# Kernel optimization log

Hardware: AMD Instinct MI355X
Metric: run time of the kernel (lower is better)

Reference implementation:

```python
import jax, jax.numpy as jnp
import numpy as np

N, F_IN, H, C, G, E = 50000, 128, 4, 64, 512, 800000
NEG_SLOPE = 0.2


def setup_inputs() -> dict:
    key = jax.random.key(0)
    ks = jax.random.split(key, 12)
    s = 0.05
    return {
        "x": jax.random.normal(ks[0], (N, F_IN), jnp.float32),
        "W1": jax.random.normal(ks[1], (F_IN, H * C), jnp.float32) * s,
        "att_src1": jax.random.normal(ks[2], (H, C), jnp.float32) * s,
        "att_dst1": jax.random.normal(ks[3], (H, C), jnp.float32) * s,
        "b1": jnp.zeros((H * C,), jnp.float32),
        "W2": jax.random.normal(ks[4], (H * C, C), jnp.float32) * s,
        "att_src2": jax.random.normal(ks[5], (1, C), jnp.float32) * s,
        "att_dst2": jax.random.normal(ks[6], (1, C), jnp.float32) * s,
        "b2": jnp.zeros((C,), jnp.float32),
        "fc_w": jax.random.normal(ks[7], (C, 1), jnp.float32) * s,
        "fc_b": jnp.zeros((1,), jnp.float32),
        "edge_index": jax.random.randint(ks[8], (2, E), 0, N, dtype=jnp.int64),
        "batch": jnp.sort(jax.random.randint(ks[9], (N,), 0, G, dtype=jnp.int64)),
    }


def gat_conv(x, src, dst, W, att_src, att_dst, bias, heads, ch):
    # PyG GATConv: linear -> per-node attn halves -> per-edge leaky_relu ->
    # segment softmax over incoming edges of dst -> weighted scatter-sum.
    n = x.shape[0]
    h = (x @ W).reshape(n, heads, ch)                       # [N,H,C]
    a_s = (h * att_src[None]).sum(-1)                       # [N,H]
    a_d = (h * att_dst[None]).sum(-1)                       # [N,H]
    alpha = jax.nn.leaky_relu(a_s[src] + a_d[dst], NEG_SLOPE)  # [E,H]
    amax = jax.ops.segment_max(alpha, dst, num_segments=n)
    ex = jnp.exp(alpha - amax[dst])
    denom = jax.ops.segment_sum(ex, dst, num_segments=n)
    w = ex / (denom[dst] + 1e-16)                           # [E,H]
    msg = h[src] * w[..., None]                             # [E,H,C]
    out = jax.ops.segment_sum(msg, dst, num_segments=n)     # [N,H,C]
    return out.reshape(n, heads * ch) + bias


def reference(x, W1, att_src1, att_dst1, b1, W2, att_src2, att_dst2, b2,
              fc_w, fc_b, edge_index, batch):
    # add self-loops (PyG GATConv default)
    loops = jnp.arange(N, dtype=edge_index.dtype)
    src = jnp.concatenate([edge_index[0], loops])
    dst = jnp.concatenate([edge_index[1], loops])
    h = jax.nn.relu(gat_conv(x, src, dst, W1, att_src1, att_dst1, b1, H, C))
    h = jax.nn.relu(gat_conv(h, src, dst, W2, att_src2, att_dst2, b2, 1, C))
    cnt = jax.ops.segment_sum(jnp.ones((N,), h.dtype), batch, num_segments=G)
    pooled = jax.ops.segment_sum(h, batch, num_segments=G) / jnp.maximum(cnt, 1.0)[:, None]
    return (pooled @ fc_w + fc_b)[:, 0]                      # [G]
```

## Files before the change

kernel.cpp:

```cpp
#include <hip/hip_runtime.h>
#include <hip/hip_fp16.h>
#include <math.h>

#define NN 50000
#define FIN 128
#define HH 4
#define CC 64
#define HC (HH*CC)
#define GG 512
#define EE 800000
#define ET (EE + NN)
#define NEG_SLOPE 0.2f
#define SCAN_NB 196

typedef _Float16 half8 __attribute__((ext_vector_type(8)));
typedef _Float16 half4 __attribute__((ext_vector_type(4)));
typedef float floatx4 __attribute__((ext_vector_type(4)));

__device__ __forceinline__ float waveReduceSum(float v) {
    #pragma unroll
    for (int off = 32; off > 0; off >>= 1) v += __shfl_xor(v, off);
    return v;
}

__global__ __launch_bounds__(256) void init0_kernel(int* __restrict__ counts,
                                                    const float* __restrict__ W1,
                                                    const float* __restrict__ W2,
                                                    __half* __restrict__ W1t,
                                                    __half* __restrict__ W2t) {
    int i = blockIdx.x * 256 + threadIdx.x;
    int stride = gridDim.x * 256;
    for (int j = i; j < NN + GG; j += stride) counts[j] = 0;
    for (int j = i; j < HC * FIN; j += stride) {
        int n = j >> 7, k = j & 127;
        W1t[j] = __float2half(W1[(size_t)k * HC + n]);
    }
    for (int j = i; j < CC * HC; j += stride) {
        int n = j >> 8, k = j & 255;
        W2t[j] = __float2half(W2[(size_t)k * CC + n]);
    }
}

__global__ __launch_bounds__(256) void histcnt_kernel(const int* __restrict__ ei,
                                                      int* __restrict__ counts,
                                                      const int* __restrict__ batch,
                                                      int* __restrict__ gcnt) {
    int e = blockIdx.x * 256 + threadIdx.x;
    if (e < ET) {
        int d = (e < EE) ? ei[EE + e] : e - EE;
        atomicAdd(&counts[d], 1);
    }
    if (e < NN) atomicAdd(&gcnt[batch[e]], 1);
}

__global__ __launch_bounds__(256) void scanA_kernel(const int* __restrict__ counts,
                                                    int* __restrict__ bsum) {
    __shared__ int sh[256];
    int t = threadIdx.x;
    int i = blockIdx.x * 256 + t;
    sh[t] = (i < NN) ? counts[i] : 0;
    __syncthreads();
    #pragma unroll
    for (int off = 128; off > 0; off >>= 1) {
        if (t < off) sh[t] += sh[t + off];
        __syncthreads();
    }
    if (t == 0) bsum[blockIdx.x] = sh[0];
}

__global__ __launch_bounds__(512) void scanB_kernel(int* __restrict__ bsum,
                                                    const int* __restrict__ gcnt,
                                                    int* __restrict__ gptr) {
    __shared__ int sh[512];
    int t = threadIdx.x;
    int v = (t < SCAN_NB) ? bsum[t] : 0;
    sh[t] = v;
    __syncthreads();
    for (int off = 1; off < 512; off <<= 1) {
        int u = (t >= off) ? sh[t - off] : 0;
        __syncthreads();
        sh[t] += u;
        __syncthreads();
    }
    if (t < SCAN_NB) bsum[t] = sh[t] - v;
    __syncthreads();
    int g = gcnt[t];
    sh[t] = g;
    __syncthreads();
    for (int off = 1; off < 512; off <<= 1) {
        int u = (t >= off) ? sh[t - off] : 0;
        __syncthreads();
        sh[t] += u;
        __syncthreads();
    }
    gptr[t] = sh[t] - g;
    if (t == 511) gptr[512] = sh[t];
}

__global__ __launch_bounds__(256) void scanC_kernel(const int* __restrict__ counts,
                                                    const int* __restrict__ bsum,
                                                    int* __restrict__ rowptr,
                                                    int* __restrict__ cursor) {
    __shared__ int sh[256];
    int t = threadIdx.x;
    int i = blockIdx.x * 256 + t;
    int v = (i < NN) ? counts[i] : 0;
    sh[t] = v;
    __syncthreads();
    for (int off = 1; off < 256; off <<= 1) {
        int u = (t >= off) ? sh[t - off] : 0;
        __syncthreads();
        sh[t] += u;
        __syncthreads();
    }
    int excl = sh[t] - v + bsum[blockIdx.x];
    if (i < NN) { rowptr[i] = excl; cursor[i] = excl; }
    if (i == NN - 1) rowptr[NN] = excl + v;
}

__global__ __launch_bounds__(256) void fill_kernel(const int* __restrict__ ei,
                                                   int* __restrict__ cursor,
                                                   int* __restrict__ scsr) {
    int e = blockIdx.x * 256 + threadIdx.x;
    if (e >= ET) return;
    int s, d;
    if (e < EE) { s = ei[e]; d = ei[EE + e]; } else { s = d = e - EE; }
    int pos = atomicAdd(&cursor[d], 1);
    scsr[pos] = s;
}

__global__ __launch_bounds__(256) void gemm1_mfma_kernel(
    const float* __restrict__ x, const __half* __restrict__ W1t,
    const float* __restrict__ att_src1, const float* __restrict__ att_dst1,
    __half* __restrict__ h1, float* __restrict__ a_s1, float* __restrict__ a_d1)
{
    __shared__ __align__(16) float xs[32][FIN + 4];
    int t = threadIdx.x;
    int n0 = blockIdx.x * 32;
    #pragma unroll
    for (int i = 0; i < 4; ++i) {
        int idx = t + i * 256;
        int row = idx >> 5, c4 = idx & 31;
        int m = n0 + row; if (m >= NN) m = NN - 1;
        float4 v = *(const float4*)(x + (size_t)m * FIN + c4 * 4);
        *(float4*)&xs[row][c4 * 4] = v;
    }
    __syncthreads();

    int w = t >> 6;
    int l = t & 63;
    int nbase = n0 + (w >> 1) * 16;
    int chalf = (w & 1) * 128;
    int lm = l & 15, lb = l >> 4;
    int lrow = (w >> 1) * 16 + lm;

    half8 afrag[4];
    #pragma unroll
    for (int q = 0; q < 4; ++q) {
        float4 lo = *(const float4*)&xs[lrow][q * 32 + lb * 8];
        float4 hi = *(const float4*)&xs[lrow][q * 32 + lb * 8 + 4];
        half8 f;
        #pragma unroll
        for (int i = 0; i < 4; ++i) {
            f[i] = (_Float16)(&lo.x)[i];
            f[4 + i] = (_Float16)(&hi.x)[i];
        }
        afrag[q] = f;
    }
    floatx4 acc[8];
    #pragma unroll
    for (int tt = 0; tt < 8; ++tt) acc[tt] = (floatx4){0.f, 0.f, 0.f, 0.f};

    const __half* wt = W1t + (size_t)(chalf + lm) * FIN + lb * 8;
    #pragma unroll
    for (int tt = 0; tt < 8; ++tt) {
        const __half* wtt = wt + (size_t)tt * 16 * FIN;
        #pragma unroll
        for (int q = 0; q < 4; ++q) {
            half8 b = *(const half8*)(wtt + q * 32);
            acc[tt] = __builtin_amdgcn_mfma_f32_16x16x32_f16(afrag[q], b, acc[tt], 0, 0, 0);
        }
    }
    #pragma unroll
    for (int hh = 0; hh < 2; ++hh) {
        float as_p[4] = {0.f, 0.f, 0.f, 0.f};
        float ad_p[4] = {0.f, 0.f, 0.f, 0.f};
        #pragma unroll
        for (int tt = 0; tt < 4; ++tt) {
            int ti = hh * 4 + tt;
            int col = chalf + ti * 16 + lm;
            float asw = att_src1[col], adw = att_dst1[col];
            #pragma unroll
            for (int r = 0; r < 4; ++r) {
                int n = nbase + lb * 4 + r;
                float v = acc[ti][r];
                if (n < NN) h1[(size_t)n * HC + col] = __float2half(v);
                as_p[r] += v * asw;
                ad_p[r] += v * adw;
            }
        }
        #pragma unroll
        for (int off = 1; off < 16; off <<= 1) {
            #pragma unroll
            for (int r = 0; r < 4; ++r) {
                as_p[r] += __shfl_xor(as_p[r], off);
                ad_p[r] += __shfl_xor(ad_p[r], off);
            }
        }
        if (lm == 0) {
            int head = (chalf >> 6) + hh;
            #pragma unroll
            for (int r = 0; r < 4; ++r) {
                int n = nbase + lb * 4 + r;
                if (n < NN) { a_s1[n * HH + head] = as_p[r]; a_d1[n * HH + head] = ad_p[r]; }
            }
        }
    }
}

__global__ __launch_bounds__(256) void emsg1_kernel(
    const int* __restrict__ rowptr, const int* __restrict__ scsr,
    const float* __restrict__ a_s, const float* __restrict__ a_d,
    const half4* __restrict__ h1v, const float* __restrict__ b1,
    half4* __restrict__ out1v)
{
    int d = blockIdx.x * 4 + (threadIdx.x >> 6);
    int l = threadIdx.x & 63;
    int head = l >> 4;
    int start = rowptr[d], end = rowptr[d + 1];
    float ad = a_d[d * HH + head];
    float den = 0.f;
    float a0 = 0.f, a1 = 0.f, a2 = 0.f, a3 = 0.f;
    int j = start;
    for (; j + 3 < end; j += 4) {
        int s0 = scsr[j], s1 = scsr[j + 1], s2 = scsr[j + 2], s3 = scsr[j + 3];
        float e0 = a_s[s0 * HH + head] + ad;
        float e1 = a_s[s1 * HH + head] + ad;
        float e2 = a_s[s2 * HH + head] + ad;
        float e3 = a_s[s3 * HH + head] + ad;
        e0 = (e0 > 0.f) ? e0 : NEG_SLOPE * e0;
        e1 = (e1 > 0.f) ? e1 : NEG_SLOPE * e1;
        e2 = (e2 > 0.f) ? e2 : NEG_SLOPE * e2;
        e3 = (e3 > 0.f) ? e3 : NEG_SLOPE * e3;
        float w0 = __expf(e0), w1 = __expf(e1), w2 = __expf(e2), w3 = __expf(e3);
        half4 v0 = h1v[(size_t)s0 * 64 + l];
        half4 v1 = h1v[(size_t)s1 * 64 + l];
        half4 v2 = h1v[(size_t)s2 * 64 + l];
        half4 v3 = h1v[(size_t)s3 * 64 + l];
        den += (w0 + w1) + (w2 + w3);
        a0 += w0 * (float)v0[0] + w1 * (float)v1[0] + w2 * (float)v2[0] + w3 * (float)v3[0];
        a1 += w0 * (float)v0[1] + w1 * (float)v1[1] + w2 * (float)v2[1] + w3 * (float)v3[1];
        a2 += w0 * (float)v0[2] + w1 * (float)v1[2] + w2 * (float)v2[2] + w3 * (float)v3[2];
        a3 += w0 * (float)v0[3] + w1 * (float)v1[3] + w2 * (float)v2[3] + w3 * (float)v3[3];
    }
    for (; j < end; ++j) {
        int s0 = scsr[j];
        float e0 = a_s[s0 * HH + head] + ad;
        e0 = (e0 > 0.f) ? e0 : NEG_SLOPE * e0;
        float w0 = __expf(e0);
        half4 v0 = h1v[(size_t)s0 * 64 + l];
        den += w0;
        a0 += w0 * (float)v0[0];
        a1 += w0 * (float)v0[1];
        a2 += w0 * (float)v0[2];
        a3 += w0 * (float)v0[3];
    }
    float inv = 1.f / (den + 1e-16f);
    float4 bb = *(const float4*)(b1 + l * 4);
    float r0 = a0 * inv + bb.x; r0 = r0 > 0.f ? r0 : 0.f;
    float r1 = a1 * inv + bb.y; r1 = r1 > 0.f ? r1 : 0.f;
    float r2 = a2 * inv + bb.z; r2 = r2 > 0.f ? r2 : 0.f;
    float r3 = a3 * inv + bb.w; r3 = r3 > 0.f ? r3 : 0.f;
    half4 o;
    o[0] = (_Float16)r0; o[1] = (_Float16)r1; o[2] = (_Float16)r2; o[3] = (_Float16)r3;
    out1v[(size_t)d * 64 + l] = o;
}

__global__ __launch_bounds__(256) void gemm2_mfma_kernel(
    const __half* __restrict__ out1r, const __half* __restrict__ W2t,
    const float* __restrict__ att_src2, const float* __restrict__ att_dst2,
    __half* __restrict__ h2, float* __restrict__ a_s2, float* __restrict__ a_d2)
{
    __shared__ __align__(16) __half ys[64][HC + 8];
    int t = threadIdx.x;
    int n0 = blockIdx.x * 64;
    #pragma unroll
    for (int i = 0; i < 8; ++i) {
        int idx = t + i * 256;
        int row = idx >> 5, c8 = idx & 31;
        int m = n0 + row; if (m >= NN) m = NN - 1;
        *(half8*)&ys[row][c8 * 8] = *(const half8*)(out1r + (size_t)m * HC + c8 * 8);
    }
    __syncthreads();

    int w = t >> 6;
    int l = t & 63;
    int nbase = n0 + w * 16;
    int lm = l & 15, lb = l >> 4;
    int lrow = w * 16 + lm;

    half8 afrag[8];
    #pragma unroll
    for (int q = 0; q < 8; ++q) afrag[q] = *(const half8*)&ys[lrow][q * 32 + lb * 8];

    floatx4 acc[4];
    #pragma unroll
    for (int tt = 0; tt < 4; ++tt) acc[tt] = (floatx4){0.f, 0.f, 0.f, 0.f};

    const __half* wt = W2t + (size_t)lm * HC + lb * 8;
    #pragma unroll
    for (int tt = 0; tt < 4; ++tt) {
        const __half* wtt = wt + (size_t)tt * 16 * HC;
        #pragma unroll
        for (int q = 0; q < 8; ++q) {
            half8 b = *(const half8*)(wtt + q * 32);
            acc[tt] = __builtin_amdgcn_mfma_f32_16x16x32_f16(afrag[q], b, acc[tt], 0, 0, 0);
        }
    }
    float as_p[4] = {0.f, 0.f, 0.f, 0.f};
    float ad_p[4] = {0.f, 0.f, 0.f, 0.f};
    #pragma unroll
    for (int tt = 0; tt < 4; ++tt) {
        int col = tt * 16 + lm;
        float asw = att_src2[col], adw = att_dst2[col];
        #pragma unroll
        for (int r = 0; r < 4; ++r) {
            int n = nbase + lb * 4 + r;
            float v = acc[tt][r];
            if (n < NN) h2[(size_t)n * CC + col] = __float2half(v);
            as_p[r] += v * asw;
            ad_p[r] += v * adw;
        }
    }
    #pragma unroll
    for (int off = 1; off < 16; off <<= 1) {
        #pragma unroll
        for (int r = 0; r < 4; ++r) {
            as_p[r] += __shfl_xor(as_p[r], off);
            ad_p[r] += __shfl_xor(ad_p[r], off);
        }
    }
    if (lm == 0) {
        #pragma unroll
        for (int r = 0; r < 4; ++r) {
            int n = nbase + lb * 4 + r;
            if (n < NN) { a_s2[n] = as_p[r]; a_d2[n] = ad_p[r]; }
        }
    }
}

__global__ __launch_bounds__(256) void emsg2_kernel(
    const int* __restrict__ rowptr, const int* __restrict__ scsr,
    const float* __restrict__ a_s, const float* __restrict__ a_d,
    const half4* __restrict__ h2v, const float* __restrict__ b2,
    const float* __restrict__ fc_w, float* __restrict__ part)
{
    int d = blockIdx.x * 4 + (threadIdx.x >> 6);
    int l = threadIdx.x & 63;
    int u = l & 15;
    int es = l >> 4;
    int start = rowptr[d], end = rowptr[d + 1];
    float ad = a_d[d];
    float den = 0.f;
    float a0 = 0.f, a1 = 0.f, a2 = 0.f, a3 = 0.f;
    int j = start + es;
    for (; j + 4 < end; j += 8) {
        int sA = scsr[j], sB = scsr[j + 4];
        float eA = a_s[sA] + ad;
        float eB = a_s[sB] + ad;
        eA = (eA > 0.f) ? eA : NEG_SLOPE * eA;
        eB = (eB > 0.f) ? eB : NEG_SLOPE * eB;
        float wA = __expf(eA), wB = __expf(eB);
        half4 vA = h2v[(size_t)sA * 16 + u];
        half4 vB = h2v[(size_t)sB * 16 + u];
        den += wA + wB;
        a0 += wA * (float)vA[0] + wB * (float)vB[0];
        a1 += wA * (float)vA[1] + wB * (float)vB[1];
        a2 += wA * (float)vA[2] + wB * (float)vB[2];
        a3 += wA * (float)vA[3] + wB * (float)vB[3];
    }
    if (j < end) {
        int s = scsr[j];
        float e = a_s[s] + ad;
        e = (e > 0.f) ? e : NEG_SLOPE * e;
        float w = __expf(e);
        half4 v = h2v[(size_t)s * 16 + u];
        den += w;
        a0 += w * (float)v[0];
        a1 += w * (float)v[1];
        a2 += w * (float)v[2];
        a3 += w * (float)v[3];
    }
    #pragma unroll
    for (int off = 16; off < 64; off <<= 1) {
        den += __shfl_xor(den, off);
        a0 += __shfl_xor(a0, off);
        a1 += __shfl_xor(a1, off);
        a2 += __shfl_xor(a2, off);
        a3 += __shfl_xor(a3, off);
    }
    float inv = 1.f / (den + 1e-16f);
    float4 bb = *(const float4*)(b2 + u * 4);
    float4 fw = *(const float4*)(fc_w + u * 4);
    float h0 = a0 * inv + bb.x; h0 = h0 > 0.f ? h0 : 0.f;
    float h1 = a1 * inv + bb.y; h1 = h1 > 0.f ? h1 : 0.f;
    float h2 = a2 * inv + bb.z; h2 = h2 > 0.f ? h2 : 0.f;
    float h3 = a3 * inv + bb.w; h3 = h3 > 0.f ? h3 : 0.f;
    float p = h0 * fw.x + h1 * fw.y + h2 * fw.z + h3 * fw.w;
    #pragma unroll
    for (int off = 1; off < 16; off <<= 1) p += __shfl_xor(p, off);
    if (l == 0) part[d] = p;
}

__global__ void pool_kernel(const float* __restrict__ part, const int* __restrict__ gptr,
                            const float* __restrict__ fc_b, float* __restrict__ out)
{
    int g = blockIdx.x;
    int lane = threadIdx.x;
    int start = gptr[g], end = gptr[g + 1];
    float s = 0.f;
    for (int i = start + lane; i < end; i += 64) s += part[i];
    s = waveReduceSum(s);
    if (lane == 0) out[g] = s / fmaxf((float)(end - start), 1.f) + fc_b[0];
}

extern "C" void kernel_launch(void* const* d_in, const int* in_sizes, int n_in,
                              void* d_out, int out_size, void* d_ws, size_t ws_size,
                              hipStream_t stream)
{
    const float* x        = (const float*)d_in[0];
    const float* W1       = (const float*)d_in[1];
    const float* att_src1 = (const float*)d_in[2];
    const float* att_dst1 = (const float*)d_in[3];
    const float* b1       = (const float*)d_in[4];
    const float* W2       = (const float*)d_in[5];
    const float* att_src2 = (const float*)d_in[6];
    const float* att_dst2 = (const float*)d_in[7];
    const float* b2       = (const float*)d_in[8];
    const float* fc_w     = (const float*)d_in[9];
    const float* fc_b     = (const float*)d_in[10];
    const int*   ei       = (const int*)d_in[11];
    const int*   batch    = (const int*)d_in[12];
    float* out = (float*)d_out;

    char* p = (char*)d_ws;
    __half* W1t   = (__half*)p; p += (size_t)HC * FIN * sizeof(__half);
    __half* W2t   = (__half*)p; p += (size_t)CC * HC * sizeof(__half);
    __half* h1    = (__half*)p; p += (size_t)NN * HC * sizeof(__half);
    __half* out1r = (__half*)p; p += (size_t)NN * HC * sizeof(__half);
    __half* h2    = (__half*)p; p += (size_t)NN * CC * sizeof(__half);
    float* a_s1   = (float*)p;  p += (size_t)NN * HH * sizeof(float);
    float* a_d1   = (float*)p;  p += (size_t)NN * HH * sizeof(float);
    float* a_s2   = (float*)p;  p += NN * sizeof(float);
    float* a_d2   = (float*)p;  p += NN * sizeof(float);
    float* part   = (float*)p;  p += NN * sizeof(float);
    int* counts   = (int*)p;    p += NN * sizeof(int);
    int* gcnt     = (int*)p;    p += GG * sizeof(int);
    int* rowptr   = (int*)p;    p += (NN + 1) * sizeof(int);
    int* cursor   = (int*)p;    p += NN * sizeof(int);
    int* scsr     = (int*)p;    p += ET * sizeof(int);
    int* bsum     = (int*)p;    p += SCAN_NB * sizeof(int);
    int* gptr     = (int*)p;    p += (GG + 1) * sizeof(int);

    const int EB = (ET + 255) / 256;

    init0_kernel<<<256, 256, 0, stream>>>(counts, W1, W2, W1t, W2t);
    histcnt_kernel<<<EB, 256, 0, stream>>>(ei, counts, batch, gcnt);
    scanA_kernel<<<SCAN_NB, 256, 0, stream>>>(counts, bsum);
    scanB_kernel<<<1, 512, 0, stream>>>(bsum, gcnt, gptr);
    scanC_kernel<<<SCAN_NB, 256, 0, stream>>>(counts, bsum, rowptr, cursor);
    fill_kernel<<<EB, 256, 0, stream>>>(ei, cursor, scsr);
    gemm1_mfma_kernel<<<(NN + 31) / 32, 256, 0, stream>>>(x, W1t, att_src1, att_dst1,
                                                          h1, a_s1, a_d1);
    emsg1_kernel<<<NN / 4, 256, 0, stream>>>(rowptr, scsr, a_s1, a_d1,
                                             (const half4*)h1, b1, (half4*)out1r);
    gemm2_mfma_kernel<<<(NN + 63) / 64, 256, 0, stream>>>(out1r, W2t, att_src2, att_dst2,
                                                          h2, a_s2, a_d2);
    emsg2_kernel<<<NN / 4, 256, 0, stream>>>(rowptr, scsr, a_s2, a_d2,
                                             (const half4*)h2, b2, fc_w, part);
    pool_kernel<<<GG, 64, 0, stream>>>(part, gptr, fc_b, out);
}
```

Before: 279.5 us.

## Fuse CSR fill into GEMM1 launch and deepen gather unrolling in edge kernels

New measurement: 287.3 us. 1.03x slower.

```diff
diff --git a/kernel.cpp b/kernel.cpp
--- a/kernel.cpp
+++ b/kernel.cpp
@@ -12,6 +12,8 @@
 #define ET (EE + NN)
 #define NEG_SLOPE 0.2f
 #define SCAN_NB 196
+#define GEMM1_NB 1563
+#define EB 3321
 
 typedef _Float16 half8 __attribute__((ext_vector_type(8)));
 typedef _Float16 half4 __attribute__((ext_vector_type(4)));
@@ -118,22 +120,21 @@
     if (i == NN - 1) rowptr[NN] = excl + v;
 }
 
-__global__ __launch_bounds__(256) void fill_kernel(const int* __restrict__ ei,
-                                                   int* __restrict__ cursor,
-                                                   int* __restrict__ scsr) {
-    int e = blockIdx.x * 256 + threadIdx.x;
-    if (e >= ET) return;
-    int s, d;
-    if (e < EE) { s = ei[e]; d = ei[EE + e]; } else { s = d = e - EE; }
-    int pos = atomicAdd(&cursor[d], 1);
-    scsr[pos] = s;
-}
-
-__global__ __launch_bounds__(256) void gemm1_mfma_kernel(
+__global__ __launch_bounds__(256) void fillgemm1_kernel(
+    const int* __restrict__ ei, int* __restrict__ cursor, int* __restrict__ scsr,
     const float* __restrict__ x, const __half* __restrict__ W1t,
     const float* __restrict__ att_src1, const float* __restrict__ att_dst1,
     __half* __restrict__ h1, float* __restrict__ a_s1, float* __restrict__ a_d1)
 {
+    if (blockIdx.x >= GEMM1_NB) {
+        int e = (blockIdx.x - GEMM1_NB) * 256 + threadIdx.x;
+        if (e >= ET) return;
+        int s, d;
+        if (e < EE) { s = ei[e]; d = ei[EE + e]; } else { s = d = e - EE; }
+        int pos = atomicAdd(&cursor[d], 1);
+        scsr[pos] = s;
+        return;
+    }
     __shared__ __align__(16) float xs[32][FIN + 4];
     int t = threadIdx.x;
     int n0 = blockIdx.x * 32;
@@ -232,26 +233,27 @@
     float den = 0.f;
     float a0 = 0.f, a1 = 0.f, a2 = 0.f, a3 = 0.f;
     int j = start;
-    for (; j + 3 < end; j += 4) {
-        int s0 = scsr[j], s1 = scsr[j + 1], s2 = scsr[j + 2], s3 = scsr[j + 3];
-        float e0 = a_s[s0 * HH + head] + ad;
-        float e1 = a_s[s1 * HH + head] + ad;
-        float e2 = a_s[s2 * HH + head] + ad;
-        float e3 = a_s[s3 * HH + head] + ad;
-        e0 = (e0 > 0.f) ? e0 : NEG_SLOPE * e0;
-        e1 = (e1 > 0.f) ? e1 : NEG_SLOPE * e1;
-        e2 = (e2 > 0.f) ? e2 : NEG_SLOPE * e2;
-        e3 = (e3 > 0.f) ? e3 : NEG_SLOPE * e3;
-        float w0 = __expf(e0), w1 = __expf(e1), w2 = __expf(e2), w3 = __expf(e3);
-        half4 v0 = h1v[(size_t)s0 * 64 + l];
-        half4 v1 = h1v[(size_t)s1 * 64 + l];
-        half4 v2 = h1v[(size_t)s2 * 64 + l];
-        half4 v3 = h1v[(size_t)s3 * 64 + l];
-        den += (w0 + w1) + (w2 + w3);
-        a0 += w0 * (float)v0[0] + w1 * (float)v1[0] + w2 * (float)v2[0] + w3 * (float)v3[0];
-        a1 += w0 * (float)v0[1] + w1 * (float)v1[1] + w2 * (float)v2[1] + w3 * (float)v3[1];
-        a2 += w0 * (float)v0[2] + w1 * (float)v1[2] + w2 * (float)v2[2] + w3 * (float)v3[2];
-        a3 += w0 * (float)v0[3] + w1 * (float)v1[3] + w2 * (float)v2[3] + w3 * (float)v3[3];
+    for (; j + 7 < end; j += 8) {
+        int s[8];
+        #pragma unroll
+        for (int q = 0; q < 8; ++q) s[q] = scsr[j + q];
+        float e[8];
+        #pragma unroll
+        for (int q = 0; q < 8; ++q) e[q] = a_s[s[q] * HH + head] + ad;
+        half4 v[8];
+        #pragma unroll
+        for (int q = 0; q < 8; ++q) v[q] = h1v[(size_t)s[q] * 64 + l];
+        #pragma unroll
+        for (int q = 0; q < 8; ++q) {
+            float eq = e[q];
+            eq = (eq > 0.f) ? eq : NEG_SLOPE * eq;
+            float wq = __expf(eq);
+            den += wq;
+            a0 += wq * (float)v[q][0];
+            a1 += wq * (float)v[q][1];
+            a2 += wq * (float)v[q][2];
+            a3 += wq * (float)v[q][3];
+        }
     }
     for (; j < end; ++j) {
         int s0 = scsr[j];
@@ -364,22 +366,29 @@
     float den = 0.f;
     float a0 = 0.f, a1 = 0.f, a2 = 0.f, a3 = 0.f;
     int j = start + es;
-    for (; j + 4 < end; j += 8) {
-        int sA = scsr[j], sB = scsr[j + 4];
-        float eA = a_s[sA] + ad;
-        float eB = a_s[sB] + ad;
-        eA = (eA > 0.f) ? eA : NEG_SLOPE * eA;
-        eB = (eB > 0.f) ? eB : NEG_SLOPE * eB;
-        float wA = __expf(eA), wB = __expf(eB);
-        half4 vA = h2v[(size_t)sA * 16 + u];
-        half4 vB = h2v[(size_t)sB * 16 + u];
-        den += wA + wB;
-        a0 += wA * (float)vA[0] + wB * (float)vB[0];
-        a1 += wA * (float)vA[1] + wB * (float)vB[1];
-        a2 += wA * (float)vA[2] + wB * (float)vB[2];
-        a3 += wA * (float)vA[3] + wB * (float)vB[3];
-    }
-    if (j < end) {
+    for (; j + 12 < end; j += 16) {
+        int s[4];
+        #pragma unroll
+        for (int q = 0; q < 4; ++q) s[q] = scsr[j + q * 4];
+        float e[4];
+        #pragma unroll
+        for (int q = 0; q < 4; ++q) e[q] = a_s[s[q]] + ad;
+        half4 v[4];
+        #pragma unroll
+        for (int q = 0; q < 4; ++q) v[q] = h2v[(size_t)s[q] * 16 + u];
+        #pragma unroll
+        for (int q = 0; q < 4; ++q) {
+            float eq = e[q];
+            eq = (eq > 0.f) ? eq : NEG_SLOPE * eq;
+            float wq = __expf(eq);
+            den += wq;
+            a0 += wq * (float)v[q][0];
+            a1 += wq * (float)v[q][1];
+            a2 += wq * (float)v[q][2];
+            a3 += wq * (float)v[q][3];
+        }
+    }
+    for (; j < end; j += 4) {
         int s = scsr[j];
         float e = a_s[s] + ad;
         e = (e > 0.f) ? e : NEG_SLOPE * e;
@@ -462,16 +471,14 @@
     int* bsum     = (int*)p;    p += SCAN_NB * sizeof(int);
     int* gptr     = (int*)p;    p += (GG + 1) * sizeof(int);
 
-    const int EB = (ET + 255) / 256;
-
     init0_kernel<<<256, 256, 0, stream>>>(counts, W1, W2, W1t, W2t);
     histcnt_kernel<<<EB, 256, 0, stream>>>(ei, counts, batch, gcnt);
     scanA_kernel<<<SCAN_NB, 256, 0, stream>>>(counts, bsum);
     scanB_kernel<<<1, 512, 0, stream>>>(bsum, gcnt, gptr);
     scanC_kernel<<<SCAN_NB, 256, 0, stream>>>(counts, bsum, rowptr, cursor);
-    fill_kernel<<<EB, 256, 0, stream>>>(ei, cursor, scsr);
-    gemm1_mfma_kernel<<<(NN + 31) / 32, 256, 0, stream>>>(x, W1t, att_src1, att_dst1,
-                                                          h1, a_s1, a_d1);
+    fillgemm1_kernel<<<GEMM1_NB + EB, 256, 0, stream>>>(ei, cursor, scsr,
+                                                        x, W1t, att_src1, att_dst1,
+                                                        h1, a_s1, a_d1);
     emsg1_kernel<<<NN / 4, 256, 0, stream>>>(rowptr, scsr, a_s1, a_d1,
                                              (const half4*)h1, b1, (half4*)out1r);
     gemm2_mfma_kernel<<<(NN + 63) / 64, 256, 0, stream>>>(out1r, W2t, att_src2, att_dst2,
```

## Merge CSR-build preprocessing kernels into one cooperative kernel with grid syncs

Applied to the files above, without the earlier changes.

After: 752.6 us. 2.69x slower.

```diff
diff --git a/kernel.cpp b/kernel.cpp
--- a/kernel.cpp
+++ b/kernel.cpp
@@ -1,6 +1,9 @@
 #include <hip/hip_runtime.h>
 #include <hip/hip_fp16.h>
+#include <hip/hip_cooperative_groups.h>
 #include <math.h>
+
+namespace cg = cooperative_groups;
 
 #define NN 50000
 #define FIN 128
@@ -12,6 +15,7 @@
 #define ET (EE + NN)
 #define NEG_SLOPE 0.2f
 #define SCAN_NB 196
+#define PREP_NB 1024
 
 typedef _Float16 half8 __attribute__((ext_vector_type(8)));
 typedef _Float16 half4 __attribute__((ext_vector_type(4)));
@@ -23,110 +27,102 @@
     return v;
 }
 
-__global__ __launch_bounds__(256) void init0_kernel(int* __restrict__ counts,
-                                                    const float* __restrict__ W1,
-                                                    const float* __restrict__ W2,
-                                                    __half* __restrict__ W1t,
-                                                    __half* __restrict__ W2t) {
-    int i = blockIdx.x * 256 + threadIdx.x;
-    int stride = gridDim.x * 256;
-    for (int j = i; j < NN + GG; j += stride) counts[j] = 0;
-    for (int j = i; j < HC * FIN; j += stride) {
+__global__ __launch_bounds__(256) void prep_kernel(
+    const int* __restrict__ ei, const int* __restrict__ batch,
+    const float* __restrict__ W1, const float* __restrict__ W2,
+    __half* __restrict__ W1t, __half* __restrict__ W2t,
+    int* __restrict__ counts, int* __restrict__ gcnt,
+    int* __restrict__ bsum, int* __restrict__ rowptr,
+    int* __restrict__ cursor, int* __restrict__ scsr, int* __restrict__ gptr)
+{
+    cg::grid_group grid = cg::this_grid();
+    __shared__ int sh[256];
+    const int t = threadIdx.x;
+    const int tid = blockIdx.x * 256 + t;
+    const int stride = PREP_NB * 256;
+
+    for (int j = tid; j < NN + GG; j += stride) counts[j] = 0;
+    for (int j = tid; j < HC * FIN; j += stride) {
         int n = j >> 7, k = j & 127;
         W1t[j] = __float2half(W1[(size_t)k * HC + n]);
     }
-    for (int j = i; j < CC * HC; j += stride) {
+    for (int j = tid; j < CC * HC; j += stride) {
         int n = j >> 8, k = j & 255;
         W2t[j] = __float2half(W2[(size_t)k * CC + n]);
     }
-}
-
-__global__ __launch_bounds__(256) void histcnt_kernel(const int* __restrict__ ei,
-                                                      int* __restrict__ counts,
-                                                      const int* __restrict__ batch,
-                                                      int* __restrict__ gcnt) {
-    int e = blockIdx.x * 256 + threadIdx.x;
-    if (e < ET) {
+    grid.sync();
+
+    for (int e = tid; e < ET; e += stride) {
         int d = (e < EE) ? ei[EE + e] : e - EE;
         atomicAdd(&counts[d], 1);
     }
-    if (e < NN) atomicAdd(&gcnt[batch[e]], 1);
-}
-
-__global__ __launch_bounds__(256) void scanA_kernel(const int* __restrict__ counts,
-                                                    int* __restrict__ bsum) {
-    __shared__ int sh[256];
-    int t = threadIdx.x;
-    int i = blockIdx.x * 256 + t;
-    sh[t] = (i < NN) ? counts[i] : 0;
-    __syncthreads();
-    #pragma unroll
-    for (int off = 128; off > 0; off >>= 1) {
-        if (t < off) sh[t] += sh[t + off];
+    for (int e = tid; e < NN; e += stride) atomicAdd(&gcnt[batch[e]], 1);
+    grid.sync();
+
+    if (blockIdx.x < SCAN_NB) {
+        int i = blockIdx.x * 256 + t;
+        sh[t] = (i < NN) ? counts[i] : 0;
         __syncthreads();
-    }
-    if (t == 0) bsum[blockIdx.x] = sh[0];
-}
-
-__global__ __launch_bounds__(512) void scanB_kernel(int* __restrict__ bsum,
-                                                    const int* __restrict__ gcnt,
-                                                    int* __restrict__ gptr) {
-    __shared__ int sh[512];
-    int t = threadIdx.x;
-    int v = (t < SCAN_NB) ? bsum[t] : 0;
-    sh[t] = v;
-    __syncthreads();
-    for (int off = 1; off < 512; off <<= 1) {
-        int u = (t >= off) ? sh[t - off] : 0;
+        #pragma unroll
+        for (int off = 128; off > 0; off >>= 1) {
+            if (t < off) sh[t] += sh[t + off];
+            __syncthreads();
+        }
+        if (t == 0) bsum[blockIdx.x] = sh[0];
+    }
+    grid.sync();
+
+    if (blockIdx.x == 0) {
+        int v = (t < SCAN_NB) ? bsum[t] : 0;
+        sh[t] = v;
         __syncthreads();
-        sh[t] += u;
+        for (int off = 1; off < 256; off <<= 1) {
+            int u = (t >= off) ? sh[t - off] : 0;
+            __syncthreads();
+            sh[t] += u;
+            __syncthreads();
+        }
+        if (t < SCAN_NB) bsum[t] = sh[t] - v;
+    } else if (blockIdx.x == 1) {
+        int g0 = gcnt[2 * t], g1 = gcnt[2 * t + 1];
+        sh[t] = g0 + g1;
         __syncthreads();
-    }
-    if (t < SCAN_NB) bsum[t] = sh[t] - v;
-    __syncthreads();
-    int g = gcnt[t];
-    sh[t] = g;
-    __syncthreads();
-    for (int off = 1; off < 512; off <<= 1) {
-        int u = (t >= off) ? sh[t - off] : 0;
+        for (int off = 1; off < 256; off <<= 1) {
+            int u = (t >= off) ? sh[t - off] : 0;
+            __syncthreads();
+            sh[t] += u;
+            __syncthreads();
+        }
+        int base = sh[t] - (g0 + g1);
+        gptr[2 * t] = base;
+        gptr[2 * t + 1] = base + g0;
+        if (t == 255) gptr[512] = sh[255];
+    }
+    grid.sync();
+
+    if (blockIdx.x < SCAN_NB) {
+        int i = blockIdx.x * 256 + t;
+        int v = (i < NN) ? counts[i] : 0;
+        sh[t] = v;
         __syncthreads();
-        sh[t] += u;
-        __syncthreads();
-    }
-    gptr[t] = sh[t] - g;
-    if (t == 511) gptr[512] = sh[t];
-}
-
-__global__ __launch_bounds__(256) void scanC_kernel(const int* __restrict__ counts,
-                                                    const int* __restrict__ bsum,
-                                                    int* __restrict__ rowptr,
-                                                    int* __restrict__ cursor) {
-    __shared__ int sh[256];
-    int t = threadIdx.x;
-    int i = blockIdx.x * 256 + t;
-    int v = (i < NN) ? counts[i] : 0;
-    sh[t] = v;
-    __syncthreads();
-    for (int off = 1; off < 256; off <<= 1) {
-        int u = (t >= off) ? sh[t - off] : 0;
-        __syncthreads();
-        sh[t] += u;
-        __syncthreads();
-    }
-    int excl = sh[t] - v + bsum[blockIdx.x];
-    if (i < NN) { rowptr[i] = excl; cursor[i] = excl; }
-    if (i == NN - 1) rowptr[NN] = excl + v;
-}
-
-__global__ __launch_bounds__(256) void fill_kernel(const int* __restrict__ ei,
-                                                   int* __restrict__ cursor,
-                                                   int* __restrict__ scsr) {
-    int e = blockIdx.x * 256 + threadIdx.x;
-    if (e >= ET) return;
-    int s, d;
-    if (e < EE) { s = ei[e]; d = ei[EE + e]; } else { s = d = e - EE; }
-    int pos = atomicAdd(&cursor[d], 1);
-    scsr[pos] = s;
+        for (int off = 1; off < 256; off <<= 1) {
+            int u = (t >= off) ? sh[t - off] : 0;
+            __syncthreads();
+            sh[t] += u;
+            __syncthreads();
+        }
+        int excl = sh[t] - v + bsum[blockIdx.x];
+        if (i < NN) { rowptr[i] = excl; cursor[i] = excl; }
+        if (i == NN - 1) rowptr[NN] = excl + v;
+    }
+    grid.sync();
+
+    for (int e = tid; e < ET; e += stride) {
+        int s, d;
+        if (e < EE) { s = ei[e]; d = ei[EE + e]; } else { s = d = e - EE; }
+        int pos = atomicAdd(&cursor[d], 1);
+        scsr[pos] = s;
+    }
 }
 
 __global__ __launch_bounds__(256) void gemm1_mfma_kernel(
@@ -462,14 +458,13 @@
     int* bsum     = (int*)p;    p += SCAN_NB * sizeof(int);
     int* gptr     = (int*)p;    p += (GG + 1) * sizeof(int);
 
-    const int EB = (ET + 255) / 256;
-
-    init0_kernel<<<256, 256, 0, stream>>>(counts, W1, W2, W1t, W2t);
-    histcnt_kernel<<<EB, 256, 0, stream>>>(ei, counts, batch, gcnt);
-    scanA_kernel<<<SCAN_NB, 256, 0, stream>>>(counts, bsum);
-    scanB_kernel<<<1, 512, 0, stream>>>(bsum, gcnt, gptr);
-    scanC_kernel<<<SCAN_NB, 256, 0, stream>>>(counts, bsum, rowptr, cursor);
-    fill_kernel<<<EB, 256, 0, stream>>>(ei, cursor, scsr);
+    void* prep_args[] = {
+        (void*)&ei, (void*)&batch, (void*)&W1, (void*)&W2,
+        (void*)&W1t, (void*)&W2t, (void*)&counts, (void*)&gcnt,
+        (void*)&bsum, (void*)&rowptr, (void*)&cursor, (void*)&scsr, (void*)&gptr
+    };
+    hipLaunchCooperativeKernel((void*)prep_kernel, dim3(PREP_NB), dim3(256),
+                               prep_args, 0, stream);
     gemm1_mfma_kernel<<<(NN + 31) / 32, 256, 0, stream>>>(x, W1t, att_src1, att_dst1,
                                                           h1, a_s1, a_d1);
     emsg1_kernel<<<NN / 4, 256, 0, stream>>>(rowptr, scsr, a_s1, a_d1,
```
